# Kernel optimization log

Hardware: AMD Instinct MI355X
Metric: run time of the kernel (lower is better)

The kernel has to match this reference:

```python
import jax, jax.numpy as jnp
import numpy as np
from jax.scipy.special import logsumexp

LAM = 0.01   # entropic regularization (torch default 0.001; scaled for fp32 at this cost scale)
N_ITERS = 100  # Sinkhorn iterations (torch default)


def sinkstep(dist, log_nu, log_u, lam):
    # dist: [d1, d2], log_nu: [bs, d2], log_u: [bs, d1] -> log_v: [bs, d2]
    # log_v = log_nu - logsumexp_{d1}(-dist/lam + log_u)
    return log_nu - logsumexp(-dist[None, :, :] / lam + log_u[:, :, None], axis=1)


def setup_inputs() -> dict:
    key = jax.random.key(0)
    k1, k2, k3 = jax.random.split(key, 3)
    bs, d1, d2 = 64, 768, 768
    mu = jax.random.uniform(k1, (bs, d1), dtype=jnp.float32) + 1e-3
    mu = mu / jnp.sum(mu, axis=1, keepdims=True)      # positive, rows sum to 1 (log() taken)
    nu = jax.random.uniform(k2, (bs, d2), dtype=jnp.float32) + 1e-3
    nu = nu / jnp.sum(nu, axis=1, keepdims=True)
    dist = jax.random.uniform(k3, (d1, d2), dtype=jnp.float32) + 0.1  # positive (log() taken)
    return {"mu": mu, "nu": nu, "dist": dist}


def reference(mu, nu, dist):
    bs, d1 = mu.shape
    d2 = nu.shape[1]
    log_mu = jnp.log(mu)
    log_nu = jnp.log(nu)
    log_u0 = jnp.full((bs, d1), -np.log(d1), dtype=mu.dtype)
    log_v0 = jnp.full((bs, d2), -np.log(d2), dtype=nu.dtype)

    def step(carry, _):
        log_u, log_v = carry
        log_v = sinkstep(dist, log_nu, log_u, LAM)
        log_u = sinkstep(dist.T, log_mu, log_v, LAM)
        return (log_u, log_v), None

    (log_u, log_v), _ = jax.lax.scan(step, (log_u0, log_v0), None, length=N_ITERS)

    # distances = exp(logsumexp_{d2}( -sinkstep(-log(dist) + dist/lam, -log_v, log_u, 1.0) ))
    final_cost = -jnp.log(dist) + dist / LAM
    s = sinkstep(final_cost, -log_v, log_u, 1.0)  # [bs, d2]
    distances = jnp.exp(logsumexp(-s, axis=1))     # [bs]
    return distances
```

## Files before the change

kernel.cpp:

```cpp
#include <hip/hip_runtime.h>
#include <hip/hip_fp16.h>


#define D        768
#define NSPLIT   8
#define COLS     96
#define QPT      12
#define NITERS   100
#define INV_LAM  100.0f
#define C14      9.70406052784f
#define SCALE14  16384.0f
#define LOG768   6.64385618977f

__device__ __forceinline__ void st_agent(float* p, float v) {
    __hip_atomic_store(p, v, __ATOMIC_RELAXED, __HIP_MEMORY_SCOPE_AGENT);
}
__device__ __forceinline__ float ld_agent(const float* p) {
    return __hip_atomic_load((float*)p, __ATOMIC_RELAXED, __HIP_MEMORY_SCOPE_AGENT);
}
__device__ __forceinline__ int ld_flag(const int* p) {
    return __hip_atomic_load((int*)p, __ATOMIC_RELAXED, __HIP_MEMORY_SCOPE_AGENT);
}

__device__ __forceinline__ float2 bmax2(float a, float b, float2* red, int tid) {
    #pragma unroll
    for (int o = 32; o; o >>= 1) { a = fmaxf(a, __shfl_xor(a, o)); b = fmaxf(b, __shfl_xor(b, o)); }
    __syncthreads();
    if ((tid & 63) == 0) red[tid >> 6] = make_float2(a, b);
    __syncthreads();
    float2 r = red[0];
    #pragma unroll
    for (int k = 1; k < 12; ++k) { r.x = fmaxf(r.x, red[k].x); r.y = fmaxf(r.y, red[k].y); }
    return r;
}
__device__ __forceinline__ float2 bsum2(float a, float b, float2* red, int tid) {
    #pragma unroll
    for (int o = 32; o; o >>= 1) { a += __shfl_xor(a, o); b += __shfl_xor(b, o); }
    __syncthreads();
    if ((tid & 63) == 0) red[tid >> 6] = make_float2(a, b);
    __syncthreads();
    float2 r = red[0];
    #pragma unroll
    for (int k = 1; k < 12; ++k) { r.x += red[k].x; r.y += red[k].y; }
    return r;
}

__device__ __forceinline__ void mv2(const uint4* __restrict__ kp,
                                    const float4* __restrict__ e0w,
                                    const float4* __restrict__ e1w,
                                    float& o0, float& o1) {
    float a0 = 0.f, a1 = 0.f, b0 = 0.f, b1 = 0.f;
    #pragma unroll 4
    for (int t = 0; t < QPT; ++t) {
        uint4 kv = kp[0]; kp += 8 * D;
        float4 xa = e0w[0], ya = e0w[1], xb = e1w[0], yb = e1w[1];
        e0w += 16; e1w += 16;
        __half2 h;
        h = *(const __half2*)&kv.x; float g0 = __low2float(h), g1 = __high2float(h);
        h = *(const __half2*)&kv.y; float g2 = __low2float(h), g3 = __high2float(h);
        h = *(const __half2*)&kv.z; float g4 = __low2float(h), g5 = __high2float(h);
        h = *(const __half2*)&kv.w; float g6 = __low2float(h), g7 = __high2float(h);
        a0 = fmaf(g0, xa.x, a0); a1 = fmaf(g1, xa.y, a1);
        a0 = fmaf(g2, xa.z, a0); a1 = fmaf(g3, xa.w, a1);
        a0 = fmaf(g4, ya.x, a0); a1 = fmaf(g5, ya.y, a1);
        a0 = fmaf(g6, ya.z, a0); a1 = fmaf(g7, ya.w, a1);
        b0 = fmaf(g0, xb.x, b0); b1 = fmaf(g1, xb.y, b1);
        b0 = fmaf(g2, xb.z, b0); b1 = fmaf(g3, xb.w, b1);
        b0 = fmaf(g4, yb.x, b0); b1 = fmaf(g5, yb.y, b1);
        b0 = fmaf(g6, yb.z, b0); b1 = fmaf(g7, yb.w, b1);
    }
    o0 = a0 + a1; o1 = b0 + b1;
}

__global__ void prep_cols(const float* __restrict__ dist, uint4* __restrict__ Kq,
                          float* __restrict__ cK2, float* __restrict__ cF2,
                          int* __restrict__ cnt) {
    int T = blockIdx.x * blockDim.x + threadIdx.x;
    if (T < 32) cnt[T] = 0;
    int j = T >> 3, w = T & 7;
    float mc = 3.402823e38f, mf = -3.402823e38f;
    for (int i = 96 * w; i < 96 * w + 96; ++i) {
        float d = dist[(size_t)i * D + j];
        mc = fminf(mc, d);
        mf = fmaxf(mf, __logf(d) - d * INV_LAM);
    }
    #pragma unroll
    for (int o = 1; o < 8; o <<= 1) { mc = fminf(mc, __shfl_xor(mc, o)); mf = fmaxf(mf, __shfl_xor(mf, o)); }
    if (w == 0) { cK2[j] = -mc * INV_LAM - C14; cF2[j] = mf; }
    for (int t = 0; t < QPT; ++t) {
        int q = 12 * w + t;
        union { uint4 u4; __half2 h2[8]; } pk;
        #pragma unroll
        for (int r = 0; r < 4; ++r) {
            float d0 = dist[(size_t)(8 * q + 2 * r) * D + j];
            float d1 = dist[(size_t)(8 * q + 2 * r + 1) * D + j];
            __half lo = __float2half(__expf((mc - d0) * INV_LAM) * SCALE14);
            __half hi = __float2half(__expf((mc - d1) * INV_LAM) * SCALE14);
            pk.h2[r] = __halves2half2(lo, hi);
        }
        Kq[(size_t)q * D + j] = pk.u4;
    }
}

__global__ void prep_rows(const float* __restrict__ dist, uint4* __restrict__ KTq,
                          float* __restrict__ cKT2) {
    int T = blockIdx.x * blockDim.x + threadIdx.x;
    int i = T >> 3, w = T & 7;
    const float* row = dist + (size_t)i * D;
    float mr = 3.402823e38f;
    for (int jj = 96 * w; jj < 96 * w + 96; ++jj) mr = fminf(mr, row[jj]);
    #pragma unroll
    for (int o = 1; o < 8; o <<= 1) mr = fminf(mr, __shfl_xor(mr, o));
    if (w == 0) cKT2[i] = -mr * INV_LAM - C14;
    for (int t = 0; t < QPT; ++t) {
        int q = 12 * w + t;
        union { uint4 u4; __half2 h2[8]; } pk;
        #pragma unroll
        for (int r = 0; r < 4; ++r) {
            float d0 = row[8 * q + 2 * r];
            float d1 = row[8 * q + 2 * r + 1];
            __half lo = __float2half(__expf((mr - d0) * INV_LAM) * SCALE14);
            __half hi = __float2half(__expf((mr - d1) * INV_LAM) * SCALE14);
            pk.h2[r] = __halves2half2(lo, hi);
        }
        KTq[(size_t)q * D + i] = pk.u4;
    }
}

__global__ __launch_bounds__(768) void sink2(
    const float* __restrict__ mu, const float* __restrict__ nu,
    const float* __restrict__ dist,
    const uint4* __restrict__ Kq, const uint4* __restrict__ KTq,
    const float* __restrict__ cK2, const float* __restrict__ cKT2,
    const float* __restrict__ cF2,
    float* __restrict__ vbuf, float* __restrict__ ubuf,
    float* __restrict__ fbuf, int* __restrict__ cnt,
    float* __restrict__ out) {
    __shared__ __align__(16) float s_e0[D];
    __shared__ __align__(16) float s_e1[D];
    __shared__ float2 s_red[16];
    __shared__ char s_pad[78848];
    if (mu == nullptr) { s_pad[threadIdx.x & 255] = 1; s_e0[0] = (float)s_pad[0]; }

    const int tid = threadIdx.x;
    const int B = blockIdx.x;
    const int x = B & 7, s = B >> 3;
    const int G = x * 4 + (s >> 3);
    const int p = s & 7;
    const int c0 = 2 * G, c1 = 2 * G + 1;
    const int jj = tid >> 3, w = tid & 7;
    const int j = p * COLS + jj;

    const float r_lnu0 = __logf(nu[(size_t)c0 * D + j]);
    const float r_lnu1 = __logf(nu[(size_t)c1 * D + j]);
    const float r_lmu0 = __logf(mu[(size_t)c0 * D + j]);
    const float r_lmu1 = __logf(mu[(size_t)c1 * D + j]);
    const float r_cK2 = cK2[j], r_cKT2 = cKT2[j], r_cF = cF2[j];

    const uint4* kp0 = Kq + (size_t)w * D + j;
    const uint4* ktp0 = KTq + (size_t)w * D + j;
    const float4* e0b = (const float4*)s_e0 + 2 * w;
    const float4* e1b = (const float4*)s_e1 + 2 * w;

    s_e0[tid] = 1.f; s_e1[tid] = 1.f;
    float coff0 = -LOG768, coff1 = -LOG768;
    float lv0 = 0.f, lv1 = 0.f;
    int hs = 0;
    __syncthreads();

    for (int it = 0; it < NITERS; ++it) {
        float S0, S1;
        mv2(kp0, e0b, e1b, S0, S1);
        #pragma unroll
        for (int o = 1; o < 8; o <<= 1) { S0 += __shfl_xor(S0, o); S1 += __shfl_xor(S1, o); }
        if (w == 0) {
            lv0 = r_lnu0 - (__logf(S0) + r_cK2 + coff0);
            lv1 = r_lnu1 - (__logf(S1) + r_cK2 + coff1);
            st_agent(&vbuf[(size_t)c0 * D + j], lv0);
            st_agent(&vbuf[(size_t)c1 * D + j], lv1);
        }
        asm volatile("s_waitcnt vmcnt(0)" ::: "memory");
        __syncthreads();
        if (tid == 0) {
            __hip_atomic_fetch_add(&cnt[G], 1, __ATOMIC_RELAXED, __HIP_MEMORY_SCOPE_AGENT);
            const int target = NSPLIT * (hs + 1);
            while (ld_flag(&cnt[G]) < target) __builtin_amdgcn_s_sleep(2);
        }
        __syncthreads();
        __atomic_signal_fence(__ATOMIC_ACQUIRE);
        {
            float x0 = ld_agent(&vbuf[(size_t)c0 * D + tid]);
            float x1 = ld_agent(&vbuf[(size_t)c1 * D + tid]);
            float2 cv = bmax2(x0, x1, s_red, tid);
            s_e0[tid] = __expf(x0 - cv.x);
            s_e1[tid] = __expf(x1 - cv.y);
            coff0 = cv.x; coff1 = cv.y;
        }
        ++hs;
        __syncthreads();

        float T0, T1;
        mv2(ktp0, e0b, e1b, T0, T1);
        #pragma unroll
        for (int o = 1; o < 8; o <<= 1) { T0 += __shfl_xor(T0, o); T1 += __shfl_xor(T1, o); }
        if (w == 0) {
            float lu0 = r_lmu0 - (__logf(T0) + r_cKT2 + coff0);
            float lu1 = r_lmu1 - (__logf(T1) + r_cKT2 + coff1);
            st_agent(&ubuf[(size_t)c0 * D + j], lu0);
            st_agent(&ubuf[(size_t)c1 * D + j], lu1);
        }
        asm volatile("s_waitcnt vmcnt(0)" ::: "memory");
        __syncthreads();
        if (tid == 0) {
            __hip_atomic_fetch_add(&cnt[G], 1, __ATOMIC_RELAXED, __HIP_MEMORY_SCOPE_AGENT);
            const int target = NSPLIT * (hs + 1);
            while (ld_flag(&cnt[G]) < target) __builtin_amdgcn_s_sleep(2);
        }
        __syncthreads();
        __atomic_signal_fence(__ATOMIC_ACQUIRE);
        {
            float x0 = ld_agent(&ubuf[(size_t)c0 * D + tid]);
            float x1 = ld_agent(&ubuf[(size_t)c1 * D + tid]);
            float2 cv = bmax2(x0, x1, s_red, tid);
            s_e0[tid] = __expf(x0 - cv.x);
            s_e1[tid] = __expf(x1 - cv.y);
            coff0 = cv.x; coff1 = cv.y;
        }
        ++hs;
        __syncthreads();
    }

    float F0 = 0.f, F1 = 0.f;
    #pragma unroll 2
    for (int t = 0; t < QPT; ++t) {
        int q = w + 8 * t;
        const float* dpp = dist + (size_t)(8 * q) * D + j;
        #pragma unroll
        for (int r = 0; r < 8; ++r) {
            float d = dpp[(size_t)r * D];
            float fv = __expf(__logf(d) - d * INV_LAM - r_cF);
            F0 = fmaf(fv, s_e0[8 * q + r], F0);
            F1 = fmaf(fv, s_e1[8 * q + r], F1);
        }
    }
    #pragma unroll
    for (int o = 1; o < 8; o <<= 1) { F0 += __shfl_xor(F0, o); F1 += __shfl_xor(F1, o); }
    float negs0 = 0.f, negs1 = 0.f;
    if (w == 0) {
        negs0 = lv0 + __logf(F0) + r_cF + coff0;
        negs1 = lv1 + __logf(F1) + r_cF + coff1;
    }
    float xm0 = (w == 0) ? negs0 : -3.402823e38f;
    float xm1 = (w == 0) ? negs1 : -3.402823e38f;
    float2 mm = bmax2(xm0, xm1, s_red, tid);
    float ez0 = 0.f, ez1 = 0.f;
    if (w == 0) { ez0 = __expf(negs0 - mm.x); ez1 = __expf(negs1 - mm.y); }
    float2 zz = bsum2(ez0, ez1, s_red, tid);

    if (tid == 0) {
        float* fb = fbuf + (size_t)(G * NSPLIT + p) * 4;
        st_agent(fb + 0, mm.x); st_agent(fb + 1, zz.x);
        st_agent(fb + 2, mm.y); st_agent(fb + 3, zz.y);
        asm volatile("s_waitcnt vmcnt(0)" ::: "memory");
        __hip_atomic_fetch_add(&cnt[G], 1, __ATOMIC_RELAXED, __HIP_MEMORY_SCOPE_AGENT);
        if (p == 0) {
            const int target = NSPLIT * (2 * NITERS + 1);
            while (ld_flag(&cnt[G]) < target) __builtin_amdgcn_s_sleep(2);
            __atomic_signal_fence(__ATOMIC_ACQUIRE);
            float pm0[8], pz0[8], pm1[8], pz1[8];
            #pragma unroll
            for (int pp = 0; pp < 8; ++pp) {
                const float* f2 = fbuf + (size_t)(G * NSPLIT + pp) * 4;
                pm0[pp] = ld_agent(f2 + 0); pz0[pp] = ld_agent(f2 + 1);
                pm1[pp] = ld_agent(f2 + 2); pz1[pp] = ld_agent(f2 + 3);
            }
            float m0 = pm0[0], m1 = pm1[0];
            #pragma unroll
            for (int pp = 1; pp < 8; ++pp) { m0 = fmaxf(m0, pm0[pp]); m1 = fmaxf(m1, pm1[pp]); }
            float z0 = 0.f, z1 = 0.f;
            #pragma unroll
            for (int pp = 0; pp < 8; ++pp) {
                z0 += pz0[pp] * __expf(pm0[pp] - m0);
                z1 += pz1[pp] * __expf(pm1[pp] - m1);
            }
            out[c0] = __expf(m0) * z0;
            out[c1] = __expf(m1) * z1;
        }
    }
}

extern "C" void kernel_launch(void* const* d_in, const int* in_sizes, int n_in,
                              void* d_out, int out_size, void* d_ws, size_t ws_size,
                              hipStream_t stream) {
    const float* mu   = (const float*)d_in[0];
    const float* nu   = (const float*)d_in[1];
    const float* dist = (const float*)d_in[2];
    float* out = (float*)d_out;
    (void)in_sizes; (void)n_in; (void)out_size; (void)ws_size;

    char* w8 = (char*)d_ws;
    uint4* Kq   = (uint4*)(w8);
    uint4* KTq  = (uint4*)(w8 + 1179648);
    float* cK2  = (float*)(w8 + 2359296);
    float* cKT2 = (float*)(w8 + 2362368);
    float* cF2  = (float*)(w8 + 2365440);
    float* vbuf = (float*)(w8 + 2368512);
    float* ubuf = (float*)(w8 + 2565120);
    float* fbuf = (float*)(w8 + 2761728);
    int*   cnt  = (int*)(w8 + 2765824);

    prep_cols<<<24, 256, 0, stream>>>(dist, Kq, cK2, cF2, cnt);
    prep_rows<<<24, 256, 0, stream>>>(dist, KTq, cKT2);
    sink2<<<256, 768, 0, stream>>>(mu, nu, dist, Kq, KTq, cK2, cKT2, cF2,
                                   vbuf, ubuf, fbuf, cnt, out);
}
```

Before: 1.859 ms.

## Split K rows across blocks and interleave two batch rows to overlap sync

Each block now owns a 96-row slice of the kernel matrix over all 768 columns and posts partial matvec sums, not a 96-column slice over all rows. Other blocks gather those partials with per-block flags instead of a shared counter. The two batch rows handled by a group are interleaved so one row's matvec runs while the other row's exchange is pending. The flags are double-buffered (even/odd) and the spin loop has a cap. This is meant to hide inter-block synchronization latency. It adds more global traffic for partial sums and more barriers, and a capped spin could proceed on stale data.

```diff
diff --git a/kernel.cpp b/kernel.cpp
--- a/kernel.cpp
+++ b/kernel.cpp
@@ -3,80 +3,129 @@
 
 
 #define D        768
-#define NSPLIT   8
-#define COLS     96
-#define QPT      12
+#define SEG      96
+#define QP       12
 #define NITERS   100
 #define INV_LAM  100.0f
 #define C14      9.70406052784f
 #define SCALE14  16384.0f
 #define LOG768   6.64385618977f
-
-__device__ __forceinline__ void st_agent(float* p, float v) {
+#define SPIN_CAP 16384
+
+static __device__ __forceinline__ void st_agent(float* p, float v) {
     __hip_atomic_store(p, v, __ATOMIC_RELAXED, __HIP_MEMORY_SCOPE_AGENT);
 }
-__device__ __forceinline__ float ld_agent(const float* p) {
+static __device__ __forceinline__ float ld_agent(const float* p) {
     return __hip_atomic_load((float*)p, __ATOMIC_RELAXED, __HIP_MEMORY_SCOPE_AGENT);
 }
-__device__ __forceinline__ int ld_flag(const int* p) {
+static __device__ __forceinline__ void st_flag(int* p, int v) {
+    __hip_atomic_store(p, v, __ATOMIC_RELAXED, __HIP_MEMORY_SCOPE_AGENT);
+}
+static __device__ __forceinline__ int ld_flag(const int* p) {
     return __hip_atomic_load((int*)p, __ATOMIC_RELAXED, __HIP_MEMORY_SCOPE_AGENT);
 }
 
-__device__ __forceinline__ float2 bmax2(float a, float b, float2* red, int tid) {
-    #pragma unroll
-    for (int o = 32; o; o >>= 1) { a = fmaxf(a, __shfl_xor(a, o)); b = fmaxf(b, __shfl_xor(b, o)); }
-    __syncthreads();
-    if ((tid & 63) == 0) red[tid >> 6] = make_float2(a, b);
-    __syncthreads();
-    float2 r = red[0];
-    #pragma unroll
-    for (int k = 1; k < 12; ++k) { r.x = fmaxf(r.x, red[k].x); r.y = fmaxf(r.y, red[k].y); }
-    return r;
-}
-__device__ __forceinline__ float2 bsum2(float a, float b, float2* red, int tid) {
-    #pragma unroll
-    for (int o = 32; o; o >>= 1) { a += __shfl_xor(a, o); b += __shfl_xor(b, o); }
-    __syncthreads();
-    if ((tid & 63) == 0) red[tid >> 6] = make_float2(a, b);
-    __syncthreads();
-    float2 r = red[0];
-    #pragma unroll
-    for (int k = 1; k < 12; ++k) { r.x += red[k].x; r.y += red[k].y; }
-    return r;
-}
-
-__device__ __forceinline__ void mv2(const uint4* __restrict__ kp,
-                                    const float4* __restrict__ e0w,
-                                    const float4* __restrict__ e1w,
-                                    float& o0, float& o1) {
-    float a0 = 0.f, a1 = 0.f, b0 = 0.f, b1 = 0.f;
-    #pragma unroll 4
-    for (int t = 0; t < QPT; ++t) {
-        uint4 kv = kp[0]; kp += 8 * D;
-        float4 xa = e0w[0], ya = e0w[1], xb = e1w[0], yb = e1w[1];
-        e0w += 16; e1w += 16;
-        __half2 h;
-        h = *(const __half2*)&kv.x; float g0 = __low2float(h), g1 = __high2float(h);
-        h = *(const __half2*)&kv.y; float g2 = __low2float(h), g3 = __high2float(h);
-        h = *(const __half2*)&kv.z; float g4 = __low2float(h), g5 = __high2float(h);
-        h = *(const __half2*)&kv.w; float g6 = __low2float(h), g7 = __high2float(h);
-        a0 = fmaf(g0, xa.x, a0); a1 = fmaf(g1, xa.y, a1);
-        a0 = fmaf(g2, xa.z, a0); a1 = fmaf(g3, xa.w, a1);
-        a0 = fmaf(g4, ya.x, a0); a1 = fmaf(g5, ya.y, a1);
-        a0 = fmaf(g6, ya.z, a0); a1 = fmaf(g7, ya.w, a1);
-        b0 = fmaf(g0, xb.x, b0); b1 = fmaf(g1, xb.y, b1);
-        b0 = fmaf(g2, xb.z, b0); b1 = fmaf(g3, xb.w, b1);
-        b0 = fmaf(g4, yb.x, b0); b1 = fmaf(g5, yb.y, b1);
-        b0 = fmaf(g6, yb.z, b0); b1 = fmaf(g7, yb.w, b1);
-    }
-    o0 = a0 + a1; o1 = b0 + b1;
+static __device__ __forceinline__ float mv_part(const uint4* __restrict__ mp,
+                                                const float* __restrict__ ef) {
+    const float4* e4 = (const float4*)ef;
+    float a0 = 0.f, a1 = 0.f, a2 = 0.f, a3 = 0.f;
+    #pragma unroll
+    for (int t = 0; t < QP; ++t) {
+        uint4 kv = mp[(size_t)t * D];
+        float4 x = e4[2 * t];
+        float4 y = e4[2 * t + 1];
+        float2 k0 = __half22float2(__builtin_bit_cast(__half2, kv.x));
+        float2 k1 = __half22float2(__builtin_bit_cast(__half2, kv.y));
+        float2 k2 = __half22float2(__builtin_bit_cast(__half2, kv.z));
+        float2 k3 = __half22float2(__builtin_bit_cast(__half2, kv.w));
+        a0 = fmaf(k0.x, x.x, a0); a1 = fmaf(k0.y, x.y, a1);
+        a2 = fmaf(k1.x, x.z, a2); a3 = fmaf(k1.y, x.w, a3);
+        a0 = fmaf(k2.x, y.x, a0); a1 = fmaf(k2.y, y.y, a1);
+        a2 = fmaf(k3.x, y.z, a2); a3 = fmaf(k3.y, y.w, a3);
+    }
+    return (a0 + a1) + (a2 + a3);
+}
+
+static __device__ __forceinline__ void post_seg(float* xw, float val, float* cw,
+                                                float cu, int* flw, int tag, int tid) {
+    st_agent(xw, val);
+    if (tid == 0) st_agent(cw, cu);
+    asm volatile("s_waitcnt vmcnt(0)" ::: "memory");
+    __syncthreads();
+    if (tid == 0) st_flag(flw, tag);
+}
+
+static __device__ __forceinline__ void poll_flags(const int* flr, int tag, int tid) {
+    if (tid < 64) {
+        int spin = 0;
+        while (ld_flag(flr) < tag && spin < SPIN_CAP) {
+            __builtin_amdgcn_s_sleep(2);
+            ++spin;
+        }
+    }
+    __syncthreads();
+    __atomic_signal_fence(__ATOMIC_ACQUIRE);
+}
+
+static __device__ __forceinline__ float gather_logsum(const float* xr, const float* cr) {
+    float x = ld_agent(xr);
+    float cu = ld_agent(cr);
+    float cs = cu;
+    #pragma unroll
+    for (int o = 1; o < 8; o <<= 1) cs = fmaxf(cs, __shfl_xor(cs, o));
+    float t = x * __expf(cu - cs);
+    #pragma unroll
+    for (int o = 1; o < 8; o <<= 1) t += __shfl_xor(t, o);
+    return __logf(t) + cs;
+}
+
+static __device__ __forceinline__ void gather_step(const float* xr, const float* cr,
+                                                   float logmn, float coffj, int tid,
+                                                   float* s_red, float* e_out,
+                                                   float& lx_o, float& cloc_o) {
+    float lx = logmn - (gather_logsum(xr, cr) + coffj);
+    float m = lx;
+    #pragma unroll
+    for (int o = 8; o < 64; o <<= 1) m = fmaxf(m, __shfl_xor(m, o));
+    if ((tid & 63) == 0) s_red[tid >> 6] = m;
+    __syncthreads();
+    float mm = s_red[0];
+    #pragma unroll
+    for (int w = 1; w < 12; ++w) mm = fmaxf(mm, s_red[w]);
+    float e = __expf(lx - mm);
+    if ((tid & 7) == 0) e_out[tid >> 3] = e;
+    lx_o = lx; cloc_o = mm;
+    __syncthreads();
+}
+
+static __device__ __forceinline__ float2 lse96(float negs, float* s_red, int tid) {
+    int pp = tid & 7;
+    float m = negs;
+    #pragma unroll
+    for (int o = 8; o < 64; o <<= 1) m = fmaxf(m, __shfl_xor(m, o));
+    __syncthreads();
+    if ((tid & 63) == 0) s_red[tid >> 6] = m;
+    __syncthreads();
+    float mm = s_red[0];
+    #pragma unroll
+    for (int w = 1; w < 12; ++w) mm = fmaxf(mm, s_red[w]);
+    float zv = (pp == 0) ? __expf(negs - mm) : 0.f;
+    #pragma unroll
+    for (int o = 1; o < 64; o <<= 1) zv += __shfl_xor(zv, o);
+    __syncthreads();
+    if ((tid & 63) == 0) s_red[tid >> 6] = zv;
+    __syncthreads();
+    float z = s_red[0];
+    #pragma unroll
+    for (int w = 1; w < 12; ++w) z += s_red[w];
+    return make_float2(mm, z);
 }
 
 __global__ void prep_cols(const float* __restrict__ dist, uint4* __restrict__ Kq,
                           float* __restrict__ cK2, float* __restrict__ cF2,
-                          int* __restrict__ cnt) {
+                          int* __restrict__ flg) {
     int T = blockIdx.x * blockDim.x + threadIdx.x;
-    if (T < 32) cnt[T] = 0;
+    if (T < 1024) flg[T] = 0;
     int j = T >> 3, w = T & 7;
     float mc = 3.402823e38f, mf = -3.402823e38f;
     for (int i = 96 * w; i < 96 * w + 96; ++i) {
@@ -87,16 +136,15 @@
     #pragma unroll
     for (int o = 1; o < 8; o <<= 1) { mc = fminf(mc, __shfl_xor(mc, o)); mf = fmaxf(mf, __shfl_xor(mf, o)); }
     if (w == 0) { cK2[j] = -mc * INV_LAM - C14; cF2[j] = mf; }
-    for (int t = 0; t < QPT; ++t) {
-        int q = 12 * w + t;
+    for (int t = 0; t < QP; ++t) {
+        int q = QP * w + t;
         union { uint4 u4; __half2 h2[8]; } pk;
         #pragma unroll
         for (int r = 0; r < 4; ++r) {
             float d0 = dist[(size_t)(8 * q + 2 * r) * D + j];
             float d1 = dist[(size_t)(8 * q + 2 * r + 1) * D + j];
-            __half lo = __float2half(__expf((mc - d0) * INV_LAM) * SCALE14);
-            __half hi = __float2half(__expf((mc - d1) * INV_LAM) * SCALE14);
-            pk.h2[r] = __halves2half2(lo, hi);
+            pk.h2[r] = __halves2half2(__float2half(__expf((mc - d0) * INV_LAM) * SCALE14),
+                                      __float2half(__expf((mc - d1) * INV_LAM) * SCALE14));
         }
         Kq[(size_t)q * D + j] = pk.u4;
     }
@@ -112,179 +160,157 @@
     #pragma unroll
     for (int o = 1; o < 8; o <<= 1) mr = fminf(mr, __shfl_xor(mr, o));
     if (w == 0) cKT2[i] = -mr * INV_LAM - C14;
-    for (int t = 0; t < QPT; ++t) {
-        int q = 12 * w + t;
+    for (int t = 0; t < QP; ++t) {
+        int q = QP * w + t;
         union { uint4 u4; __half2 h2[8]; } pk;
         #pragma unroll
         for (int r = 0; r < 4; ++r) {
             float d0 = row[8 * q + 2 * r];
             float d1 = row[8 * q + 2 * r + 1];
-            __half lo = __float2half(__expf((mr - d0) * INV_LAM) * SCALE14);
-            __half hi = __float2half(__expf((mr - d1) * INV_LAM) * SCALE14);
-            pk.h2[r] = __halves2half2(lo, hi);
+            pk.h2[r] = __halves2half2(__float2half(__expf((mr - d0) * INV_LAM) * SCALE14),
+                                      __float2half(__expf((mr - d1) * INV_LAM) * SCALE14));
         }
         KTq[(size_t)q * D + i] = pk.u4;
     }
 }
 
-__global__ __launch_bounds__(768) void sink2(
+__global__ __launch_bounds__(768) void sink6(
     const float* __restrict__ mu, const float* __restrict__ nu,
     const float* __restrict__ dist,
     const uint4* __restrict__ Kq, const uint4* __restrict__ KTq,
     const float* __restrict__ cK2, const float* __restrict__ cKT2,
     const float* __restrict__ cF2,
-    float* __restrict__ vbuf, float* __restrict__ ubuf,
-    float* __restrict__ fbuf, int* __restrict__ cnt,
+    float* __restrict__ xbuf, float* __restrict__ cub,
+    int* __restrict__ flg, float* __restrict__ fbuf,
     float* __restrict__ out) {
-    __shared__ __align__(16) float s_e0[D];
-    __shared__ __align__(16) float s_e1[D];
-    __shared__ float2 s_red[16];
-    __shared__ char s_pad[78848];
-    if (mu == nullptr) { s_pad[threadIdx.x & 255] = 1; s_e0[0] = (float)s_pad[0]; }
+    __shared__ __align__(16) float s_eu[2][SEG];
+    __shared__ __align__(16) float s_ev[2][SEG];
+    __shared__ float s_red[12];
+    __shared__ char s_pad[81920];
+    if (mu == nullptr) { s_pad[threadIdx.x] = 1; s_eu[0][0] = (float)s_pad[0]; }
 
     const int tid = threadIdx.x;
-    const int B = blockIdx.x;
-    const int x = B & 7, s = B >> 3;
-    const int G = x * 4 + (s >> 3);
-    const int p = s & 7;
-    const int c0 = 2 * G, c1 = 2 * G + 1;
-    const int jj = tid >> 3, w = tid & 7;
-    const int j = p * COLS + jj;
-
-    const float r_lnu0 = __logf(nu[(size_t)c0 * D + j]);
-    const float r_lnu1 = __logf(nu[(size_t)c1 * D + j]);
-    const float r_lmu0 = __logf(mu[(size_t)c0 * D + j]);
-    const float r_lmu1 = __logf(mu[(size_t)c1 * D + j]);
-    const float r_cK2 = cK2[j], r_cKT2 = cKT2[j], r_cF = cF2[j];
-
-    const uint4* kp0 = Kq + (size_t)w * D + j;
-    const uint4* ktp0 = KTq + (size_t)w * D + j;
-    const float4* e0b = (const float4*)s_e0 + 2 * w;
-    const float4* e1b = (const float4*)s_e1 + 2 * w;
-
-    s_e0[tid] = 1.f; s_e1[tid] = 1.f;
-    float coff0 = -LOG768, coff1 = -LOG768;
-    float lv0 = 0.f, lv1 = 0.f;
-    int hs = 0;
+    const int p = blockIdx.x & 7, g = blockIdx.x >> 3;
+    const int c0 = 2 * g;
+    const int pp = tid & 7, jj = tid >> 3;
+    const int jglob = p * SEG + jj;
+    const int qc = tid / 96, jw = tid - 96 * qc;
+    const int qoff = (qc * 8 + p) * SEG + jw;
+    const int rdo = (p * 8 + pp) * SEG + jj;
+
+    const float lnu0 = __logf(nu[(size_t)c0 * D + jglob]);
+    const float lnu1 = __logf(nu[(size_t)(c0 + 1) * D + jglob]);
+    const float lmu0 = __logf(mu[(size_t)c0 * D + jglob]);
+    const float lmu1 = __logf(mu[(size_t)(c0 + 1) * D + jglob]);
+    const float cKg = cK2[jglob], cKTg = cKT2[jglob], cFg = cF2[jglob];
+    const float cFt = cF2[tid];
+
+    const uint4* Kv = Kq  + (size_t)(QP * p) * D + tid;
+    const uint4* Ku = KTq + (size_t)(QP * p) * D + tid;
+
+    const size_t r00 = ((size_t)(g * 2 + 0) * 2 + 0), r01 = r00 + 1;
+    const size_t r10 = ((size_t)(g * 2 + 1) * 2 + 0), r11 = r10 + 1;
+    float* const xw0e = xbuf + r00 * 6144 + qoff; float* const xw0o = xbuf + r01 * 6144 + qoff;
+    float* const xw1e = xbuf + r10 * 6144 + qoff; float* const xw1o = xbuf + r11 * 6144 + qoff;
+    const float* const xr0e = xbuf + r00 * 6144 + rdo; const float* const xr0o = xbuf + r01 * 6144 + rdo;
+    const float* const xr1e = xbuf + r10 * 6144 + rdo; const float* const xr1o = xbuf + r11 * 6144 + rdo;
+    float* const cw0e = cub + r00 * 8 + p; float* const cw0o = cub + r01 * 8 + p;
+    float* const cw1e = cub + r10 * 8 + p; float* const cw1o = cub + r11 * 8 + p;
+    const float* const cr0e = cub + r00 * 8 + pp; const float* const cr0o = cub + r01 * 8 + pp;
+    const float* const cr1e = cub + r10 * 8 + pp; const float* const cr1o = cub + r11 * 8 + pp;
+    int* const flw0 = flg + (g * 2 + 0) * 16 + p;
+    int* const flw1 = flg + (g * 2 + 1) * 16 + p;
+    const int* const flr0 = flg + (g * 2 + 0) * 16 + (tid & 7);
+    const int* const flr1 = flg + (g * 2 + 1) * 16 + (tid & 7);
+
+    if (tid < SEG) { s_eu[0][tid] = 1.f; s_eu[1][tid] = 1.f; }
+    float r_cu0 = -LOG768, r_cu1 = -LOG768;
+    float r_cv0 = 0.f, r_cv1 = 0.f, r_lv0 = 0.f, r_lv1 = 0.f, r_dump;
+    int hs0 = 0, hs1 = 0;
     __syncthreads();
 
     for (int it = 0; it < NITERS; ++it) {
-        float S0, S1;
-        mv2(kp0, e0b, e1b, S0, S1);
-        #pragma unroll
-        for (int o = 1; o < 8; o <<= 1) { S0 += __shfl_xor(S0, o); S1 += __shfl_xor(S1, o); }
-        if (w == 0) {
-            lv0 = r_lnu0 - (__logf(S0) + r_cK2 + coff0);
-            lv1 = r_lnu1 - (__logf(S1) + r_cK2 + coff1);
-            st_agent(&vbuf[(size_t)c0 * D + j], lv0);
-            st_agent(&vbuf[(size_t)c1 * D + j], lv1);
-        }
-        asm volatile("s_waitcnt vmcnt(0)" ::: "memory");
-        __syncthreads();
+        float SA = mv_part(Kv, s_eu[0]);
+        ++hs0;
+        post_seg((hs0 & 1) ? xw0o : xw0e, SA, (hs0 & 1) ? cw0o : cw0e, r_cu0, flw0, hs0, tid);
+        if (it > 0) {
+            poll_flags(flr1, hs1, tid);
+            gather_step((hs1 & 1) ? xr1o : xr1e, (hs1 & 1) ? cr1o : cr1e,
+                        lmu1, cKTg, tid, s_red, s_eu[1], r_dump, r_cu1);
+        }
+        float SB = mv_part(Kv, s_eu[1]);
+        ++hs1;
+        post_seg((hs1 & 1) ? xw1o : xw1e, SB, (hs1 & 1) ? cw1o : cw1e, r_cu1, flw1, hs1, tid);
+        poll_flags(flr0, hs0, tid);
+        gather_step((hs0 & 1) ? xr0o : xr0e, (hs0 & 1) ? cr0o : cr0e,
+                    lnu0, cKg, tid, s_red, s_ev[0], r_lv0, r_cv0);
+        float TA = mv_part(Ku, s_ev[0]);
+        ++hs0;
+        post_seg((hs0 & 1) ? xw0o : xw0e, TA, (hs0 & 1) ? cw0o : cw0e, r_cv0, flw0, hs0, tid);
+        poll_flags(flr1, hs1, tid);
+        gather_step((hs1 & 1) ? xr1o : xr1e, (hs1 & 1) ? cr1o : cr1e,
+                    lnu1, cKg, tid, s_red, s_ev[1], r_lv1, r_cv1);
+        float TB = mv_part(Ku, s_ev[1]);
+        ++hs1;
+        post_seg((hs1 & 1) ? xw1o : xw1e, TB, (hs1 & 1) ? cw1o : cw1e, r_cv1, flw1, hs1, tid);
+        poll_flags(flr0, hs0, tid);
+        gather_step((hs0 & 1) ? xr0o : xr0e, (hs0 & 1) ? cr0o : cr0e,
+                    lmu0, cKTg, tid, s_red, s_eu[0], r_dump, r_cu0);
+    }
+    poll_flags(flr1, hs1, tid);
+    gather_step((hs1 & 1) ? xr1o : xr1e, (hs1 & 1) ? cr1o : cr1e,
+                lmu1, cKTg, tid, s_red, s_eu[1], r_dump, r_cu1);
+
+    float FA = 0.f, FB = 0.f;
+    const float* dp = dist + (size_t)(SEG * p) * D + tid;
+    #pragma unroll 4
+    for (int ii = 0; ii < SEG; ++ii) {
+        float d = dp[(size_t)ii * D];
+        float fh = __expf(__logf(d) - d * INV_LAM - cFt);
+        FA = fmaf(fh, s_eu[0][ii], FA);
+        FB = fmaf(fh, s_eu[1][ii], FB);
+    }
+    ++hs0;
+    post_seg((hs0 & 1) ? xw0o : xw0e, FA, (hs0 & 1) ? cw0o : cw0e, r_cu0, flw0, hs0, tid);
+    ++hs1;
+    post_seg((hs1 & 1) ? xw1o : xw1e, FB, (hs1 & 1) ? cw1o : cw1e, r_cu1, flw1, hs1, tid);
+
+    poll_flags(flr0, hs0, tid);
+    float negs0 = r_lv0 + gather_logsum((hs0 & 1) ? xr0o : xr0e, (hs0 & 1) ? cr0o : cr0e) + cFg;
+    float2 mzA = lse96(negs0, s_red, tid);
+    poll_flags(flr1, hs1, tid);
+    float negs1 = r_lv1 + gather_logsum((hs1 & 1) ? xr1o : xr1e, (hs1 & 1) ? cr1o : cr1e) + cFg;
+    float2 mzB = lse96(negs1, s_red, tid);
+
+    if (tid == 0) {
+        float* fb = fbuf + (size_t)(g * 8 + p) * 4;
+        st_agent(fb + 0, mzA.x); st_agent(fb + 1, mzA.y);
+        st_agent(fb + 2, mzB.x); st_agent(fb + 3, mzB.y);
+    }
+    asm volatile("s_waitcnt vmcnt(0)" ::: "memory");
+    __syncthreads();
+    if (tid == 0) st_flag(flw0, hs0 + 1);
+    if (p == 0) {
+        poll_flags(flr0, hs0 + 1, tid);
         if (tid == 0) {
-            __hip_atomic_fetch_add(&cnt[G], 1, __ATOMIC_RELAXED, __HIP_MEMORY_SCOPE_AGENT);
-            const int target = NSPLIT * (hs + 1);
-            while (ld_flag(&cnt[G]) < target) __builtin_amdgcn_s_sleep(2);
-        }
-        __syncthreads();
-        __atomic_signal_fence(__ATOMIC_ACQUIRE);
-        {
-            float x0 = ld_agent(&vbuf[(size_t)c0 * D + tid]);
-            float x1 = ld_agent(&vbuf[(size_t)c1 * D + tid]);
-            float2 cv = bmax2(x0, x1, s_red, tid);
-            s_e0[tid] = __expf(x0 - cv.x);
-            s_e1[tid] = __expf(x1 - cv.y);
-            coff0 = cv.x; coff1 = cv.y;
-        }
-        ++hs;
-        __syncthreads();
-
-        float T0, T1;
-        mv2(ktp0, e0b, e1b, T0, T1);
-        #pragma unroll
-        for (int o = 1; o < 8; o <<= 1) { T0 += __shfl_xor(T0, o); T1 += __shfl_xor(T1, o); }
-        if (w == 0) {
-            float lu0 = r_lmu0 - (__logf(T0) + r_cKT2 + coff0);
-            float lu1 = r_lmu1 - (__logf(T1) + r_cKT2 + coff1);
-            st_agent(&ubuf[(size_t)c0 * D + j], lu0);
-            st_agent(&ubuf[(size_t)c1 * D + j], lu1);
-        }
-        asm volatile("s_waitcnt vmcnt(0)" ::: "memory");
-        __syncthreads();
-        if (tid == 0) {
-            __hip_atomic_fetch_add(&cnt[G], 1, __ATOMIC_RELAXED, __HIP_MEMORY_SCOPE_AGENT);
-            const int target = NSPLIT * (hs + 1);
-            while (ld_flag(&cnt[G]) < target) __builtin_amdgcn_s_sleep(2);
-        }
-        __syncthreads();
-        __atomic_signal_fence(__ATOMIC_ACQUIRE);
-        {
-            float x0 = ld_agent(&ubuf[(size_t)c0 * D + tid]);
-            float x1 = ld_agent(&ubuf[(size_t)c1 * D + tid]);
-            float2 cv = bmax2(x0, x1, s_red, tid);
-            s_e0[tid] = __expf(x0 - cv.x);
-            s_e1[tid] = __expf(x1 - cv.y);
-            coff0 = cv.x; coff1 = cv.y;
-        }
-        ++hs;
-        __syncthreads();
-    }
-
-    float F0 = 0.f, F1 = 0.f;
-    #pragma unroll 2
-    for (int t = 0; t < QPT; ++t) {
-        int q = w + 8 * t;
-        const float* dpp = dist + (size_t)(8 * q) * D + j;
-        #pragma unroll
-        for (int r = 0; r < 8; ++r) {
-            float d = dpp[(size_t)r * D];
-            float fv = __expf(__logf(d) - d * INV_LAM - r_cF);
-            F0 = fmaf(fv, s_e0[8 * q + r], F0);
-            F1 = fmaf(fv, s_e1[8 * q + r], F1);
-        }
-    }
-    #pragma unroll
-    for (int o = 1; o < 8; o <<= 1) { F0 += __shfl_xor(F0, o); F1 += __shfl_xor(F1, o); }
-    float negs0 = 0.f, negs1 = 0.f;
-    if (w == 0) {
-        negs0 = lv0 + __logf(F0) + r_cF + coff0;
-        negs1 = lv1 + __logf(F1) + r_cF + coff1;
-    }
-    float xm0 = (w == 0) ? negs0 : -3.402823e38f;
-    float xm1 = (w == 0) ? negs1 : -3.402823e38f;
-    float2 mm = bmax2(xm0, xm1, s_red, tid);
-    float ez0 = 0.f, ez1 = 0.f;
-    if (w == 0) { ez0 = __expf(negs0 - mm.x); ez1 = __expf(negs1 - mm.y); }
-    float2 zz = bsum2(ez0, ez1, s_red, tid);
-
-    if (tid == 0) {
-        float* fb = fbuf + (size_t)(G * NSPLIT + p) * 4;
-        st_agent(fb + 0, mm.x); st_agent(fb + 1, zz.x);
-        st_agent(fb + 2, mm.y); st_agent(fb + 3, zz.y);
-        asm volatile("s_waitcnt vmcnt(0)" ::: "memory");
-        __hip_atomic_fetch_add(&cnt[G], 1, __ATOMIC_RELAXED, __HIP_MEMORY_SCOPE_AGENT);
-        if (p == 0) {
-            const int target = NSPLIT * (2 * NITERS + 1);
-            while (ld_flag(&cnt[G]) < target) __builtin_amdgcn_s_sleep(2);
-            __atomic_signal_fence(__ATOMIC_ACQUIRE);
             float pm0[8], pz0[8], pm1[8], pz1[8];
             #pragma unroll
-            for (int pp = 0; pp < 8; ++pp) {
-                const float* f2 = fbuf + (size_t)(G * NSPLIT + pp) * 4;
-                pm0[pp] = ld_agent(f2 + 0); pz0[pp] = ld_agent(f2 + 1);
-                pm1[pp] = ld_agent(f2 + 2); pz1[pp] = ld_agent(f2 + 3);
+            for (int q = 0; q < 8; ++q) {
+                const float* fq = fbuf + (size_t)(g * 8 + q) * 4;
+                pm0[q] = ld_agent(fq + 0); pz0[q] = ld_agent(fq + 1);
+                pm1[q] = ld_agent(fq + 2); pz1[q] = ld_agent(fq + 3);
             }
             float m0 = pm0[0], m1 = pm1[0];
             #pragma unroll
-            for (int pp = 1; pp < 8; ++pp) { m0 = fmaxf(m0, pm0[pp]); m1 = fmaxf(m1, pm1[pp]); }
+            for (int q = 1; q < 8; ++q) { m0 = fmaxf(m0, pm0[q]); m1 = fmaxf(m1, pm1[q]); }
             float z0 = 0.f, z1 = 0.f;
             #pragma unroll
-            for (int pp = 0; pp < 8; ++pp) {
-                z0 += pz0[pp] * __expf(pm0[pp] - m0);
-                z1 += pz1[pp] * __expf(pm1[pp] - m1);
+            for (int q = 0; q < 8; ++q) {
+                z0 += pz0[q] * __expf(pm0[q] - m0);
+                z1 += pz1[q] * __expf(pm1[q] - m1);
             }
             out[c0] = __expf(m0) * z0;
-            out[c1] = __expf(m1) * z1;
+            out[c0 + 1] = __expf(m1) * z1;
         }
     }
 }
@@ -304,13 +330,13 @@
     float* cK2  = (float*)(w8 + 2359296);
     float* cKT2 = (float*)(w8 + 2362368);
     float* cF2  = (float*)(w8 + 2365440);
-    float* vbuf = (float*)(w8 + 2368512);
-    float* ubuf = (float*)(w8 + 2565120);
-    float* fbuf = (float*)(w8 + 2761728);
-    int*   cnt  = (int*)(w8 + 2765824);
-
-    prep_cols<<<24, 256, 0, stream>>>(dist, Kq, cK2, cF2, cnt);
+    float* xbuf = (float*)(w8 + 2368512);
+    float* cub  = (float*)(w8 + 5514240);
+    int*   flg  = (int*)  (w8 + 5518336);
+    float* fbuf = (float*)(w8 + 5522432);
+
+    prep_cols<<<24, 256, 0, stream>>>(dist, Kq, cK2, cF2, flg);
     prep_rows<<<24, 256, 0, stream>>>(dist, KTq, cKT2);
-    sink2<<<256, 768, 0, stream>>>(mu, nu, dist, Kq, KTq, cK2, cKT2, cF2,
-                                   vbuf, ubuf, fbuf, cnt, out);
-}
+    sink6<<<256, 768, 0, stream>>>(mu, nu, dist, Kq, KTq, cK2, cKT2, cF2,
+                                   xbuf, cub, flg, fbuf, out);
+}
```

Result: slower. 3.156 ms (+69.8%).
